# Performance work log

Hardware: AMD Instinct MI355X
Metric: run time of the kernel (lower is better)

The kernel has to match this reference:

```python
import jax, jax.numpy as jnp
import numpy as np
from functools import partial

H = 128  # GRU hidden size
L = 16   # dim_latents


def _gru_dir(x_tbd, W_ih, W_hh, b_ih, b_hh):
    """Single-direction GRU over time-major input x_tbd [T,B,D] -> [T,B,H].
    Torch gate order: r, z, n."""
    T, B, _ = x_tbd.shape
    # Precompute input projections for all timesteps: [T,B,3H]
    xp = jnp.einsum('tbd,gd->tbg', x_tbd, W_ih) + b_ih
    h0 = jnp.zeros((B, H), dtype=x_tbd.dtype)

    def step(h, xp_t):
        gh = h @ W_hh.T + b_hh            # [B,3H]
        xr, xz, xn = jnp.split(xp_t, 3, axis=-1)
        hr, hz, hn = jnp.split(gh, 3, axis=-1)
        r = jax.nn.sigmoid(xr + hr)
        z = jax.nn.sigmoid(xz + hz)
        n = jnp.tanh(xn + r * hn)
        h_new = (1.0 - z) * n + z * h
        return h_new, h_new

    _, ys = jax.lax.scan(step, h0, xp)
    return ys  # [T,B,H]


def setup_inputs() -> dict:
    key = jax.random.key(0)
    ks = jax.random.split(key, 8)
    B, T, N = 256, 1000, 256
    s_ih = 1.0 / np.sqrt(N)
    s_hh = 1.0 / np.sqrt(H)
    s_fc = 1.0 / np.sqrt(2 * H + L)
    return {
        'y_aux': jax.random.normal(ks[0], (B, T, N), dtype=jnp.float32),
        'W_ih_fwd': jax.random.normal(ks[1], (3 * H, N), dtype=jnp.float32) * s_ih,
        'W_hh_fwd': jax.random.normal(ks[2], (3 * H, H), dtype=jnp.float32) * s_hh,
        'b_ih_fwd': jnp.zeros((3 * H,), dtype=jnp.float32),
        'b_hh_fwd': jnp.zeros((3 * H,), dtype=jnp.float32),
        'W_ih_bwd': jax.random.normal(ks[3], (3 * H, N), dtype=jnp.float32) * s_ih,
        'W_hh_bwd': jax.random.normal(ks[4], (3 * H, H), dtype=jnp.float32) * s_hh,
        'b_ih_bwd': jnp.zeros((3 * H,), dtype=jnp.float32),
        'b_hh_bwd': jnp.zeros((3 * H,), dtype=jnp.float32),
        'W_mu': jax.random.normal(ks[5], (L, 2 * H + L), dtype=jnp.float32) * s_fc,
        'b_mu': jnp.zeros((L,), dtype=jnp.float32),
        'W_lv': jax.random.normal(ks[6], (L, 2 * H + L), dtype=jnp.float32) * s_fc,
        'b_lv': jnp.zeros((L,), dtype=jnp.float32),
    }


def reference(y_aux, W_ih_fwd, W_hh_fwd, b_ih_fwd, b_hh_fwd,
              W_ih_bwd, W_hh_bwd, b_ih_bwd, b_hh_bwd,
              W_mu, b_mu, W_lv, b_lv):
    # [B,T,N] -> time-major [T,B,N]
    x = jnp.transpose(y_aux, (1, 0, 2))
    out_f = _gru_dir(x, W_ih_fwd, W_hh_fwd, b_ih_fwd, b_hh_fwd)
    out_b = _gru_dir(x[::-1], W_ih_bwd, W_hh_bwd, b_ih_bwd, b_hh_bwd)[::-1]
    rnn_output = jnp.concatenate([out_f, out_b], axis=-1)  # [T,B,2H]
    # hn[0]: bidirectional hidden states at t=0
    hn0 = rnn_output[0]                                    # [B,2H]
    B = hn0.shape[0]
    temp = jnp.concatenate([jnp.zeros((B, L), dtype=hn0.dtype), hn0], axis=1)
    mu_0 = temp @ W_mu.T + b_mu
    log_var_0 = temp @ W_lv.T + b_lv
    return (mu_0, log_var_0, rnn_output)
```

## Files before the change

### kernel.cpp

```cpp
#include <hip/hip_runtime.h>
#include <hip/hip_bf16.h>

typedef short bf16x8 __attribute__((ext_vector_type(8)));
typedef float f32x4  __attribute__((ext_vector_type(4)));

#define TSTEPS 1000
#define BATCH  256
#define NIN    256
#define HID    128
#define TC     25
#define XP_T_STRIDE 98304ll
#define XP_NEED (2ull*TSTEPS*XP_T_STRIDE*2ull)

__device__ __forceinline__ ushort f2bf(float f){
  union { float f; unsigned u; } v; v.f = f;
  unsigned r = v.u + 0x7fffu + ((v.u >> 16) & 1u);
  return (ushort)(r >> 16);
}
__device__ __forceinline__ uint pk2(float lo, float hi){
  __hip_bfloat162 h = __float22bfloat162_rn(make_float2(lo, hi));
  union { __hip_bfloat162 h; uint u; } c; c.h = h; return c.u;
}
__device__ __forceinline__ float bflo(uint w){ union{uint u;float f;}c; c.u = w<<16; return c.f; }
__device__ __forceinline__ float bfhi(uint w){ union{uint u;float f;}c; c.u = w & 0xffff0000u; return c.f; }

__device__ __forceinline__ float sigmoid_fast(float x){
  return __builtin_amdgcn_rcpf(1.f + __expf(-x));
}
__device__ __forceinline__ float tanh_fast(float a){
  const float e = __expf(2.f*fabsf(a));
  const float t = fmaf(-2.f, __builtin_amdgcn_rcpf(e + 1.f), 1.f);
  return copysignf(t, a);
}
__device__ __forceinline__ bf16x8 ld_w8(const float* p){
  union { uint u[4]; bf16x8 v; } c;
  c.u[0]=pk2(p[0],p[1]); c.u[1]=pk2(p[2],p[3]);
  c.u[2]=pk2(p[4],p[5]); c.u[3]=pk2(p[6],p[7]);
  return c.v;
}

__global__ __launch_bounds__(512) void xp_gemm(
    const float* __restrict__ y_aux,
    const float* __restrict__ Wf, const float* __restrict__ bihf, const float* __restrict__ bhhf,
    const float* __restrict__ Wb, const float* __restrict__ bihb, const float* __restrict__ bhhb,
    ushort* __restrict__ xp)
{
  const int nch = TSTEPS/TC;
  const int blk = blockIdx.x;
  const int dir = blk / (16*nch);
  const int rem = blk % (16*nch);
  const int btile = rem / nch;
  const int tch = rem % nch;
  const int b0 = btile*16;
  const int tid=threadIdx.x, wave=tid>>6, lane=tid&63, lrow=lane&15, lgrp=lane>>4;
  const float* Wih = dir? Wb : Wf;
  const float* bih = dir? bihb : bihf;
  const float* bhh = dir? bhhb : bhhf;

  __shared__ __align__(16) ushort xsh[2][16][264];

  bf16x8 wf[3][8];
  float bias[3];
  #pragma unroll
  for (int t3=0;t3<3;++t3){
    const int g = t3*128 + wave*16 + lrow;
    #pragma unroll
    for (int kk=0;kk<8;++kk)
      wf[t3][kk] = ld_w8(Wih + g*NIN + kk*32 + lgrp*8);
    bias[t3] = bih[g] + (t3<2 ? bhh[g] : 0.f);
  }

  const int row = tid>>5, f8 = tid&31;
  const float* xsrc = y_aux + (size_t)(b0+row)*(TSTEPS*NIN) + (size_t)(tch*TC)*NIN + f8*8;
  {
    float4 a = *(const float4*)xsrc;
    float4 b = *(const float4*)(xsrc+4);
    union{uint u[4]; bf16x8 v;} c;
    c.u[0]=pk2(a.x,a.y); c.u[1]=pk2(a.z,a.w); c.u[2]=pk2(b.x,b.y); c.u[3]=pk2(b.z,b.w);
    *(bf16x8*)&xsh[0][row][f8*8] = c.v;
  }
  __syncthreads();

  ushort* sp = xp + (size_t)dir*TSTEPS*XP_T_STRIDE + (size_t)(tch*TC)*XP_T_STRIDE
             + ((size_t)((btile*8 + wave)*64 + lane))*12;

  for (int k=0;k<TC;++k){
    const int cur=k&1, nxt=cur^1;
    const bool more = (k < TC-1);
    float4 pa, pb;
    if (more){
      const float* p = xsrc + (size_t)(k+1)*NIN;
      pa = *(const float4*)p;
      pb = *(const float4*)(p+4);
    }
    f32x4 a0={0,0,0,0}, a1={0,0,0,0}, a2={0,0,0,0};
    #pragma unroll
    for (int kk=0;kk<8;++kk){
      bf16x8 a = *(const bf16x8*)&xsh[cur][lrow][kk*32 + lgrp*8];
      a0 = __builtin_amdgcn_mfma_f32_16x16x32_bf16(a, wf[0][kk], a0, 0,0,0);
      a1 = __builtin_amdgcn_mfma_f32_16x16x32_bf16(a, wf[1][kk], a1, 0,0,0);
      a2 = __builtin_amdgcn_mfma_f32_16x16x32_bf16(a, wf[2][kk], a2, 0,0,0);
    }
    const uint d0=pk2(a0[0]+bias[0], a0[1]+bias[0]);
    const uint d1=pk2(a0[2]+bias[0], a0[3]+bias[0]);
    const uint d2=pk2(a1[0]+bias[1], a1[1]+bias[1]);
    const uint d3=pk2(a1[2]+bias[1], a1[3]+bias[1]);
    const uint d4=pk2(a2[0]+bias[2], a2[1]+bias[2]);
    const uint d5=pk2(a2[2]+bias[2], a2[3]+bias[2]);
    *(uint2*)(sp)   = make_uint2(d0,d1);
    *(uint2*)(sp+4) = make_uint2(d2,d3);
    *(uint2*)(sp+8) = make_uint2(d4,d5);
    sp += XP_T_STRIDE;
    if (more){
      union{uint u[4]; bf16x8 v;} c;
      c.u[0]=pk2(pa.x,pa.y); c.u[1]=pk2(pa.z,pa.w); c.u[2]=pk2(pb.x,pb.y); c.u[3]=pk2(pb.z,pb.w);
      *(bf16x8*)&xsh[nxt][row][f8*8] = c.v;
    }
    asm volatile("s_waitcnt lgkmcnt(0)\n\ts_barrier" ::: "memory");
  }
}

__global__ __launch_bounds__(512) void gru_rec(
    const ushort* __restrict__ xp,
    const float* __restrict__ Whhf, const float* __restrict__ bhhf,
    const float* __restrict__ Whhb, const float* __restrict__ bhhb,
    float* __restrict__ out)
{
  const int blk=blockIdx.x, dir=blk>>4, btile=blk&15, b0=btile<<4;
  const int tid=threadIdx.x, wave=tid>>6, lane=tid&63, lrow=lane&15, lgrp=lane>>4;
  const float* Whh = dir? Whhb : Whhf;
  const float* bhh = dir? bhhb : bhhf;

  __shared__ __align__(16) ushort hbuf[2][16][136];

  bf16x8 whh[3][4];
  #pragma unroll
  for (int t3=0;t3<3;++t3){
    const int g = t3*128 + wave*16 + lrow;
    #pragma unroll
    for (int kk=0;kk<4;++kk)
      whh[t3][kk] = ld_w8(Whh + g*HID + kk*32 + lgrp*8);
  }
  const int hcol = wave*16 + lrow;
  const float bh2 = bhh[256 + hcol];

  { ushort* hb=&hbuf[0][0][0]; for (int i=tid;i<16*136;i+=512) hb[i]=0; }

  const int tt0 = dir? (TSTEPS-1):0;
  const long long sdel = dir? -XP_T_STRIDE : XP_T_STRIDE;
  const ushort* xpp = xp + (size_t)dir*TSTEPS*XP_T_STRIDE + (size_t)tt0*XP_T_STRIDE
                    + ((size_t)((btile*8+wave)*64+lane))*12;
  uint2 qa = *(const uint2*)(xpp);
  uint2 qb = *(const uint2*)(xpp+4);
  uint2 qc = *(const uint2*)(xpp+8);

  float* op = out + 8192 + (size_t)tt0*(BATCH*2*HID)
            + (size_t)(b0 + lgrp*4)*(2*HID) + dir*HID + hcol;
  const long long odel = dir? -(long long)(BATCH*2*HID) : (long long)(BATCH*2*HID);

  float hm[4]={0,0,0,0};
  __syncthreads();

  for (int s=0;s<TSTEPS;++s){
    const int cur=s&1, nxt=cur^1;
    const bool more = (s<TSTEPS-1);
    const ushort* pn = xpp + sdel;
    uint2 pa_=qa, pb_=qb, pc_=qc;
    if (more){
      pa_ = *(const uint2*)(pn);
      pb_ = *(const uint2*)(pn+4);
      pc_ = *(const uint2*)(pn+8);
    }

    f32x4 ar={0,0,0,0}, az={0,0,0,0}, an={0,0,0,0};
    #pragma unroll
    for (int kk=0;kk<4;++kk){
      bf16x8 a = *(const bf16x8*)&hbuf[cur][lrow][kk*32 + lgrp*8];
      ar = __builtin_amdgcn_mfma_f32_16x16x32_bf16(a, whh[0][kk], ar, 0,0,0);
      az = __builtin_amdgcn_mfma_f32_16x16x32_bf16(a, whh[1][kk], az, 0,0,0);
      an = __builtin_amdgcn_mfma_f32_16x16x32_bf16(a, whh[2][kk], an, 0,0,0);
    }

    float hvv[4];
    {
      const float xr0=bflo(qa.x), xr1=bfhi(qa.x), xr2=bflo(qa.y), xr3=bfhi(qa.y);
      const float xz0=bflo(qb.x), xz1=bfhi(qb.x), xz2=bflo(qb.y), xz3=bfhi(qb.y);
      const float xn0=bflo(qc.x), xn1=bfhi(qc.x), xn2=bflo(qc.y), xn3=bfhi(qc.y);
      const float r0=sigmoid_fast(ar[0]+xr0), r1=sigmoid_fast(ar[1]+xr1);
      const float r2=sigmoid_fast(ar[2]+xr2), r3=sigmoid_fast(ar[3]+xr3);
      const float z0=sigmoid_fast(az[0]+xz0), z1=sigmoid_fast(az[1]+xz1);
      const float z2=sigmoid_fast(az[2]+xz2), z3=sigmoid_fast(az[3]+xz3);
      const float n0=tanh_fast(fmaf(r0, an[0]+bh2, xn0));
      const float n1=tanh_fast(fmaf(r1, an[1]+bh2, xn1));
      const float n2=tanh_fast(fmaf(r2, an[2]+bh2, xn2));
      const float n3=tanh_fast(fmaf(r3, an[3]+bh2, xn3));
      hvv[0]=n0 + z0*(hm[0]-n0); hvv[1]=n1 + z1*(hm[1]-n1);
      hvv[2]=n2 + z2*(hm[2]-n2); hvv[3]=n3 + z3*(hm[3]-n3);
    }
    hm[0]=hvv[0]; hm[1]=hvv[1]; hm[2]=hvv[2]; hm[3]=hvv[3];
    op[0*(2*HID)] = hvv[0];
    op[1*(2*HID)] = hvv[1];
    op[2*(2*HID)] = hvv[2];
    op[3*(2*HID)] = hvv[3];
    const uint p01 = pk2(hvv[0], hvv[1]);
    const uint p23 = pk2(hvv[2], hvv[3]);
    hbuf[nxt][lgrp*4+0][hcol] = (ushort)p01;
    hbuf[nxt][lgrp*4+1][hcol] = (ushort)(p01>>16);
    hbuf[nxt][lgrp*4+2][hcol] = (ushort)p23;
    hbuf[nxt][lgrp*4+3][hcol] = (ushort)(p23>>16);

    op += odel; xpp = pn; qa=pa_; qb=pb_; qc=pc_;
    asm volatile("s_waitcnt lgkmcnt(0)\n\ts_barrier" ::: "memory");
  }
}

__global__ __launch_bounds__(512) void gru_fused(
    const float* __restrict__ y_aux,
    const float* __restrict__ W_ih_f, const float* __restrict__ W_hh_f,
    const float* __restrict__ b_ih_f, const float* __restrict__ b_hh_f,
    const float* __restrict__ W_ih_b, const float* __restrict__ W_hh_b,
    const float* __restrict__ b_ih_b, const float* __restrict__ b_hh_b,
    float* __restrict__ out)
{
  const int blk  = blockIdx.x;
  const int dir  = blk >> 4;
  const int b0   = (blk & 15) << 4;
  const int tid  = threadIdx.x;
  const int wave = tid >> 6;
  const int lane = tid & 63;
  const int lrow = lane & 15;
  const int lgrp = lane >> 4;

  const float* Wih = dir ? W_ih_b : W_ih_f;
  const float* Whh = dir ? W_hh_b : W_hh_f;
  const float* bih = dir ? b_ih_b : b_ih_f;
  const float* bhh = dir ? b_hh_b : b_hh_f;

  __shared__ __align__(16) ushort hbuf[2][16][136];
  __shared__ __align__(16) ushort xbuf[2][16][264];

  bf16x8 wih_f[3][8];
  bf16x8 whh_f[3][4];
  #pragma unroll
  for (int t3 = 0; t3 < 3; ++t3){
    const int g = t3*128 + wave*16 + lrow;
    #pragma unroll
    for (int kk = 0; kk < 8; ++kk) wih_f[t3][kk] = ld_w8(Wih + g*NIN + kk*32 + lgrp*8);
    #pragma unroll
    for (int kk = 0; kk < 4; ++kk) whh_f[t3][kk] = ld_w8(Whh + g*HID + kk*32 + lgrp*8);
  }
  float bihv[3], bhhv[3];
  #pragma unroll
  for (int t3 = 0; t3 < 3; ++t3){
    const int g = t3*128 + wave*16 + lrow;
    bihv[t3] = bih[g];
    bhhv[t3] = bhh[g];
  }

  for (int i = tid; i < 2*16*136; i += 512) ((ushort*)hbuf)[i] = 0;
  {
    const int row = tid >> 5, f8 = tid & 31;
    const int t0  = dir ? (TSTEPS-1) : 0;
    const float* p = y_aux + (size_t)(b0+row)*(TSTEPS*NIN) + (size_t)t0*NIN + f8*8;
    union{uint u[4]; bf16x8 v;} c;
    float4 a = *(const float4*)p; float4 b = *(const float4*)(p+4);
    c.u[0]=pk2(a.x,a.y); c.u[1]=pk2(a.z,a.w); c.u[2]=pk2(b.x,b.y); c.u[3]=pk2(b.z,b.w);
    *(bf16x8*)&xbuf[0][row][f8*8] = c.v;
  }
  __syncthreads();

  float hm[4] = {0.f, 0.f, 0.f, 0.f};
  const int hcol = wave*16 + lrow;
  float* outr = out + 8192;

  for (int s = 0; s < TSTEPS; ++s){
    const int tt  = dir ? (TSTEPS-1-s) : s;
    const int cur = s & 1, nxt = cur ^ 1;
    const int tn   = dir ? (tt-1) : (tt+1);
    const int prow = tid >> 5, pf8 = tid & 31;
    const bool more = (s < TSTEPS-1);
    float4 pa, pb;
    if (more){
      const float* p = y_aux + (size_t)(b0+prow)*(TSTEPS*NIN) + (size_t)tn*NIN + pf8*8;
      pa = *(const float4*)p;
      pb = *(const float4*)(p+4);
    }

    f32x4 a_rh = {0,0,0,0}, a_zh = {0,0,0,0}, a_nh = {0,0,0,0};
    f32x4 a_rx = {0,0,0,0}, a_zx = {0,0,0,0}, a_nx = {0,0,0,0};
    #pragma unroll
    for (int kk = 0; kk < 4; ++kk){
      bf16x8 a = *(const bf16x8*)&hbuf[cur][lrow][kk*32 + lgrp*8];
      a_rh = __builtin_amdgcn_mfma_f32_16x16x32_bf16(a, whh_f[0][kk], a_rh, 0,0,0);
      a_zh = __builtin_amdgcn_mfma_f32_16x16x32_bf16(a, whh_f[1][kk], a_zh, 0,0,0);
      a_nh = __builtin_amdgcn_mfma_f32_16x16x32_bf16(a, whh_f[2][kk], a_nh, 0,0,0);
    }
    #pragma unroll
    for (int kk = 0; kk < 8; ++kk){
      bf16x8 a = *(const bf16x8*)&xbuf[cur][lrow][kk*32 + lgrp*8];
      a_rx = __builtin_amdgcn_mfma_f32_16x16x32_bf16(a, wih_f[0][kk], a_rx, 0,0,0);
      a_zx = __builtin_amdgcn_mfma_f32_16x16x32_bf16(a, wih_f[1][kk], a_zx, 0,0,0);
      a_nx = __builtin_amdgcn_mfma_f32_16x16x32_bf16(a, wih_f[2][kk], a_nx, 0,0,0);
    }

    #pragma unroll
    for (int i = 0; i < 4; ++i){
      const float rp  = a_rh[i] + a_rx[i] + bihv[0] + bhhv[0];
      const float zp  = a_zh[i] + a_zx[i] + bihv[1] + bhhv[1];
      const float hnp = a_nh[i] + bhhv[2];
      const float xnp = a_nx[i] + bihv[2];
      const float r = sigmoid_fast(rp);
      const float z = sigmoid_fast(zp);
      const float n = tanh_fast(fmaf(r, hnp, xnp));
      const float hv = n + z*(hm[i] - n);
      hm[i] = hv;
      outr[(size_t)tt*(BATCH*2*HID) + (size_t)(b0 + lgrp*4 + i)*(2*HID)
           + dir*HID + hcol] = hv;
      hbuf[nxt][lgrp*4 + i][hcol] = f2bf(hv);
    }

    if (more){
      union{uint u[4]; bf16x8 v;} c;
      c.u[0]=pk2(pa.x,pa.y); c.u[1]=pk2(pa.z,pa.w); c.u[2]=pk2(pb.x,pb.y); c.u[3]=pk2(pb.z,pb.w);
      *(bf16x8*)&xbuf[nxt][prow][pf8*8] = c.v;
    }
    __syncthreads();
  }
}

__global__ void heads(const float* __restrict__ out_rnn,
    const float* __restrict__ W_mu, const float* __restrict__ b_mu,
    const float* __restrict__ W_lv, const float* __restrict__ b_lv,
    float* __restrict__ out)
{
  const int oid   = blockIdx.x*256 + threadIdx.x;
  const int which = oid >> 12;
  const int r     = oid & 4095;
  const int b = r >> 4, j = r & 15;
  const float* W    = which ? W_lv : W_mu;
  const float* bias = which ? b_lv : b_mu;
  const float* h = out_rnn + b*256;
  const float* w = W + j*272 + 16;
  float acc = bias[j];
  for (int c = 0; c < 256; c += 4){
    acc += h[c]*w[c] + h[c+1]*w[c+1] + h[c+2]*w[c+2] + h[c+3]*w[c+3];
  }
  out[(which << 12) + r] = acc;
}

extern "C" void kernel_launch(void* const* d_in, const int* in_sizes, int n_in,
                              void* d_out, int out_size, void* d_ws, size_t ws_size,
                              hipStream_t stream)
{
  const float* y    = (const float*)d_in[0];
  const float* Wihf = (const float*)d_in[1];
  const float* Whhf = (const float*)d_in[2];
  const float* bihf = (const float*)d_in[3];
  const float* bhhf = (const float*)d_in[4];
  const float* Wihb = (const float*)d_in[5];
  const float* Whhb = (const float*)d_in[6];
  const float* bihb = (const float*)d_in[7];
  const float* bhhb = (const float*)d_in[8];
  const float* Wmu  = (const float*)d_in[9];
  const float* bmu  = (const float*)d_in[10];
  const float* Wlv  = (const float*)d_in[11];
  const float* blv  = (const float*)d_in[12];
  float* out = (float*)d_out;

  if (ws_size >= (size_t)XP_NEED){
    ushort* xpw = (ushort*)d_ws;
    xp_gemm<<<dim3(2*16*(TSTEPS/TC)), dim3(512), 0, stream>>>(
        y, Wihf, bihf, bhhf, Wihb, bihb, bhhb, xpw);
    gru_rec<<<dim3(32), dim3(512), 0, stream>>>(
        xpw, Whhf, bhhf, Whhb, bhhb, out);
  } else {
    gru_fused<<<dim3(32), dim3(512), 0, stream>>>(
        y, Wihf, Whhf, bihf, bhhf, Wihb, Whhb, bihb, bhhb, out);
  }
  heads<<<dim3(32), dim3(256), 0, stream>>>(out + 8192, Wmu, bmu, Wlv, blv, out);
}
```

Before: 1.117 ms.

## Prescale gates by log2e, split xp into uint4/uint2 planes, deepen prefetch

Folds log2(e) into the input-projection outputs and the recurrent weights and bias, so the recurrent loop can call exp2 directly instead of exp. The precomputed projection buffer is split into a 16-byte r/z plane and an 8-byte n plane, so each timestep needs two wide loads instead of three 8-byte loads. The recurrent kernel now prefetches two timesteps ahead to hide global-memory latency in the serial loop, and the time-chunk size of the GEMM kernel goes from 25 to 40. The costs are a changed workspace layout and slightly different rounding, because the scaled values are stored in bf16.

```diff
diff --git a/kernel.cpp b/kernel.cpp
--- a/kernel.cpp
+++ b/kernel.cpp
@@ -8,9 +8,13 @@
 #define BATCH  256
 #define NIN    256
 #define HID    128
-#define TC     25
-#define XP_T_STRIDE 98304ll
-#define XP_NEED (2ull*TSTEPS*XP_T_STRIDE*2ull)
+#define TC     40
+#define LOG2E  1.44269504088896f
+
+#define GIDX_N 8192
+#define XP4_ELEMS (2ull*TSTEPS*GIDX_N)
+#define XP2_OFF_BYTES (XP4_ELEMS*16ull)
+#define XP_NEED (XP4_ELEMS*16ull + 2ull*TSTEPS*GIDX_N*8ull)
 
 __device__ __forceinline__ ushort f2bf(float f){
   union { float f; unsigned u; } v; v.f = f;
@@ -38,12 +42,18 @@
   c.u[2]=pk2(p[4],p[5]); c.u[3]=pk2(p[6],p[7]);
   return c.v;
 }
+__device__ __forceinline__ bf16x8 ld_w8s(const float* p, float s){
+  union { uint u[4]; bf16x8 v; } c;
+  c.u[0]=pk2(p[0]*s,p[1]*s); c.u[1]=pk2(p[2]*s,p[3]*s);
+  c.u[2]=pk2(p[4]*s,p[5]*s); c.u[3]=pk2(p[6]*s,p[7]*s);
+  return c.v;
+}
 
 __global__ __launch_bounds__(512) void xp_gemm(
     const float* __restrict__ y_aux,
     const float* __restrict__ Wf, const float* __restrict__ bihf, const float* __restrict__ bhhf,
     const float* __restrict__ Wb, const float* __restrict__ bihb, const float* __restrict__ bhhb,
-    ushort* __restrict__ xp)
+    uint4* __restrict__ xp4, uint2* __restrict__ xp2)
 {
   const int nch = TSTEPS/TC;
   const int blk = blockIdx.x;
@@ -60,14 +70,14 @@
   __shared__ __align__(16) ushort xsh[2][16][264];
 
   bf16x8 wf[3][8];
-  float bias[3];
+  float biass[3];
   #pragma unroll
   for (int t3=0;t3<3;++t3){
     const int g = t3*128 + wave*16 + lrow;
     #pragma unroll
     for (int kk=0;kk<8;++kk)
       wf[t3][kk] = ld_w8(Wih + g*NIN + kk*32 + lgrp*8);
-    bias[t3] = bih[g] + (t3<2 ? bhh[g] : 0.f);
+    biass[t3] = LOG2E * (bih[g] + (t3<2 ? bhh[g] : 0.f));
   }
 
   const int row = tid>>5, f8 = tid&31;
@@ -81,8 +91,10 @@
   }
   __syncthreads();
 
-  ushort* sp = xp + (size_t)dir*TSTEPS*XP_T_STRIDE + (size_t)(tch*TC)*XP_T_STRIDE
-             + ((size_t)((btile*8 + wave)*64 + lane))*12;
+  const size_t gbase = ((size_t)dir*TSTEPS + (size_t)(tch*TC))*GIDX_N
+                     + (size_t)((btile*8 + wave)*64 + lane);
+  uint4* s4 = xp4 + gbase;
+  uint2* s2 = xp2 + gbase;
 
   for (int k=0;k<TC;++k){
     const int cur=k&1, nxt=cur^1;
@@ -101,16 +113,16 @@
       a1 = __builtin_amdgcn_mfma_f32_16x16x32_bf16(a, wf[1][kk], a1, 0,0,0);
       a2 = __builtin_amdgcn_mfma_f32_16x16x32_bf16(a, wf[2][kk], a2, 0,0,0);
     }
-    const uint d0=pk2(a0[0]+bias[0], a0[1]+bias[0]);
-    const uint d1=pk2(a0[2]+bias[0], a0[3]+bias[0]);
-    const uint d2=pk2(a1[0]+bias[1], a1[1]+bias[1]);
-    const uint d3=pk2(a1[2]+bias[1], a1[3]+bias[1]);
-    const uint d4=pk2(a2[0]+bias[2], a2[1]+bias[2]);
-    const uint d5=pk2(a2[2]+bias[2], a2[3]+bias[2]);
-    *(uint2*)(sp)   = make_uint2(d0,d1);
-    *(uint2*)(sp+4) = make_uint2(d2,d3);
-    *(uint2*)(sp+8) = make_uint2(d4,d5);
-    sp += XP_T_STRIDE;
+    uint4 o4;
+    o4.x = pk2(fmaf(LOG2E,a0[0],biass[0]), fmaf(LOG2E,a0[1],biass[0]));
+    o4.y = pk2(fmaf(LOG2E,a0[2],biass[0]), fmaf(LOG2E,a0[3],biass[0]));
+    o4.z = pk2(fmaf(LOG2E,a1[0],biass[1]), fmaf(LOG2E,a1[1],biass[1]));
+    o4.w = pk2(fmaf(LOG2E,a1[2],biass[1]), fmaf(LOG2E,a1[3],biass[1]));
+    uint2 o2;
+    o2.x = pk2(fmaf(LOG2E,a2[0],biass[2]), fmaf(LOG2E,a2[1],biass[2]));
+    o2.y = pk2(fmaf(LOG2E,a2[2],biass[2]), fmaf(LOG2E,a2[3],biass[2]));
+    *s4 = o4;  s4 += GIDX_N;
+    *s2 = o2;  s2 += GIDX_N;
     if (more){
       union{uint u[4]; bf16x8 v;} c;
       c.u[0]=pk2(pa.x,pa.y); c.u[1]=pk2(pa.z,pa.w); c.u[2]=pk2(pb.x,pb.y); c.u[3]=pk2(pb.z,pb.w);
@@ -121,7 +133,7 @@
 }
 
 __global__ __launch_bounds__(512) void gru_rec(
-    const ushort* __restrict__ xp,
+    const uint4* __restrict__ xp4, const uint2* __restrict__ xp2,
     const float* __restrict__ Whhf, const float* __restrict__ bhhf,
     const float* __restrict__ Whhb, const float* __restrict__ bhhb,
     float* __restrict__ out)
@@ -139,20 +151,23 @@
     const int g = t3*128 + wave*16 + lrow;
     #pragma unroll
     for (int kk=0;kk<4;++kk)
-      whh[t3][kk] = ld_w8(Whh + g*HID + kk*32 + lgrp*8);
+      whh[t3][kk] = ld_w8s(Whh + g*HID + kk*32 + lgrp*8, LOG2E);
   }
   const int hcol = wave*16 + lrow;
-  const float bh2 = bhh[256 + hcol];
+  const float bh2s = LOG2E * bhh[256 + hcol];
 
   { ushort* hb=&hbuf[0][0][0]; for (int i=tid;i<16*136;i+=512) hb[i]=0; }
 
   const int tt0 = dir? (TSTEPS-1):0;
-  const long long sdel = dir? -XP_T_STRIDE : XP_T_STRIDE;
-  const ushort* xpp = xp + (size_t)dir*TSTEPS*XP_T_STRIDE + (size_t)tt0*XP_T_STRIDE
-                    + ((size_t)((btile*8+wave)*64+lane))*12;
-  uint2 qa = *(const uint2*)(xpp);
-  uint2 qb = *(const uint2*)(xpp+4);
-  uint2 qc = *(const uint2*)(xpp+8);
+  const long long d4 = dir? -(long long)GIDX_N : (long long)GIDX_N;
+  const size_t gbase = ((size_t)dir*TSTEPS + (size_t)tt0)*GIDX_N
+                     + (size_t)((btile*8+wave)*64+lane);
+  const uint4* q4p = xp4 + gbase;
+  const uint2* q2p = xp2 + gbase;
+  uint4 q40 = q4p[0], q41 = q4p[d4];
+  uint2 q20 = q2p[0], q21 = q2p[d4];
+  const uint4* f4 = q4p + 2*d4;
+  const uint2* f2 = q2p + 2*d4;
 
   float* op = out + 8192 + (size_t)tt0*(BATCH*2*HID)
             + (size_t)(b0 + lgrp*4)*(2*HID) + dir*HID + hcol;
@@ -163,14 +178,8 @@
 
   for (int s=0;s<TSTEPS;++s){
     const int cur=s&1, nxt=cur^1;
-    const bool more = (s<TSTEPS-1);
-    const ushort* pn = xpp + sdel;
-    uint2 pa_=qa, pb_=qb, pc_=qc;
-    if (more){
-      pa_ = *(const uint2*)(pn);
-      pb_ = *(const uint2*)(pn+4);
-      pc_ = *(const uint2*)(pn+8);
-    }
+    uint4 q42 = *f4; f4 += d4;
+    uint2 q22 = *f2; f2 += d4;
 
     f32x4 ar={0,0,0,0}, az={0,0,0,0}, an={0,0,0,0};
     #pragma unroll
@@ -181,35 +190,36 @@
       an = __builtin_amdgcn_mfma_f32_16x16x32_bf16(a, whh[2][kk], an, 0,0,0);
     }
 
-    float hvv[4];
+    float hv[4];
     {
-      const float xr0=bflo(qa.x), xr1=bfhi(qa.x), xr2=bflo(qa.y), xr3=bfhi(qa.y);
-      const float xz0=bflo(qb.x), xz1=bfhi(qb.x), xz2=bflo(qb.y), xz3=bfhi(qb.y);
-      const float xn0=bflo(qc.x), xn1=bfhi(qc.x), xn2=bflo(qc.y), xn3=bfhi(qc.y);
-      const float r0=sigmoid_fast(ar[0]+xr0), r1=sigmoid_fast(ar[1]+xr1);
-      const float r2=sigmoid_fast(ar[2]+xr2), r3=sigmoid_fast(ar[3]+xr3);
-      const float z0=sigmoid_fast(az[0]+xz0), z1=sigmoid_fast(az[1]+xz1);
-      const float z2=sigmoid_fast(az[2]+xz2), z3=sigmoid_fast(az[3]+xz3);
-      const float n0=tanh_fast(fmaf(r0, an[0]+bh2, xn0));
-      const float n1=tanh_fast(fmaf(r1, an[1]+bh2, xn1));
-      const float n2=tanh_fast(fmaf(r2, an[2]+bh2, xn2));
-      const float n3=tanh_fast(fmaf(r3, an[3]+bh2, xn3));
-      hvv[0]=n0 + z0*(hm[0]-n0); hvv[1]=n1 + z1*(hm[1]-n1);
-      hvv[2]=n2 + z2*(hm[2]-n2); hvv[3]=n3 + z3*(hm[3]-n3);
-    }
-    hm[0]=hvv[0]; hm[1]=hvv[1]; hm[2]=hvv[2]; hm[3]=hvv[3];
-    op[0*(2*HID)] = hvv[0];
-    op[1*(2*HID)] = hvv[1];
-    op[2*(2*HID)] = hvv[2];
-    op[3*(2*HID)] = hvv[3];
-    const uint p01 = pk2(hvv[0], hvv[1]);
-    const uint p23 = pk2(hvv[2], hvv[3]);
+      const float xr[4] = {bflo(q40.x),bfhi(q40.x),bflo(q40.y),bfhi(q40.y)};
+      const float xz[4] = {bflo(q40.z),bfhi(q40.z),bflo(q40.w),bfhi(q40.w)};
+      const float xn[4] = {bflo(q20.x),bfhi(q20.x),bflo(q20.y),bfhi(q20.y)};
+      #pragma unroll
+      for (int i=0;i<4;++i){
+        const float r = __builtin_amdgcn_rcpf(1.f + __builtin_amdgcn_exp2f(-(ar[i]+xr[i])));
+        const float z = __builtin_amdgcn_rcpf(1.f + __builtin_amdgcn_exp2f(-(az[i]+xz[i])));
+        const float y  = fmaf(r, an[i]+bh2s, xn[i]);
+        const float y2 = y + y;
+        const float e  = __builtin_amdgcn_exp2f(fabsf(y2));
+        const float t  = fmaf(-2.f, __builtin_amdgcn_rcpf(e+1.f), 1.f);
+        const float n  = copysignf(t, y);
+        hv[i] = fmaf(z, hm[i]-n, n);
+        hm[i] = hv[i];
+      }
+    }
+    const uint p01 = pk2(hv[0],hv[1]);
+    const uint p23 = pk2(hv[2],hv[3]);
     hbuf[nxt][lgrp*4+0][hcol] = (ushort)p01;
     hbuf[nxt][lgrp*4+1][hcol] = (ushort)(p01>>16);
     hbuf[nxt][lgrp*4+2][hcol] = (ushort)p23;
     hbuf[nxt][lgrp*4+3][hcol] = (ushort)(p23>>16);
-
-    op += odel; xpp = pn; qa=pa_; qb=pb_; qc=pc_;
+    op[0]   = hv[0];
+    op[256] = hv[1];
+    op[512] = hv[2];
+    op[768] = hv[3];
+    op += odel;
+    q40=q41; q41=q42; q20=q21; q21=q22;
     asm volatile("s_waitcnt lgkmcnt(0)\n\ts_barrier" ::: "memory");
   }
 }
@@ -368,11 +378,12 @@
   float* out = (float*)d_out;
 
   if (ws_size >= (size_t)XP_NEED){
-    ushort* xpw = (ushort*)d_ws;
+    uint4* xp4 = (uint4*)d_ws;
+    uint2* xp2 = (uint2*)((char*)d_ws + XP2_OFF_BYTES);
     xp_gemm<<<dim3(2*16*(TSTEPS/TC)), dim3(512), 0, stream>>>(
-        y, Wihf, bihf, bhhf, Wihb, bihb, bhhb, xpw);
+        y, Wihf, bihf, bhhf, Wihb, bihb, bhhb, xp4, xp2);
     gru_rec<<<dim3(32), dim3(512), 0, stream>>>(
-        xpw, Whhf, bhhf, Whhb, bhhb, out);
+        xp4, xp2, Whhf, bhhf, Whhb, bhhb, out);
   } else {
     gru_fused<<<dim3(32), dim3(512), 0, stream>>>(
         y, Wihf, Whhf, bihf, bhhf, Wihb, Whhb, bihb, bhhb, out);
```

Result: faster. 958.7 us (-14.2%).
